# Performance work log

Hardware: AMD Instinct MI355X
Metric: run time of the kernel (lower is better)

The kernel has to match this reference:

```python
import jax, jax.numpy as jnp
import numpy as np

B, C, H, W = 16, 256, 64, 64
NUM_HEADS = 4
GROUPS = 8
EPS = 1e-5


def setup_inputs() -> dict:
    key = jax.random.key(0)
    ks = jax.random.split(key, 7)
    x = jax.random.normal(ks[0], (B, C, H, W), dtype=jnp.float32)
    # GroupNorm affine params (torch default: weight=1, bias=0; randomize slightly for a stronger test)
    norm_w = jnp.ones((C,), jnp.float32) + 0.1 * jax.random.normal(ks[1], (C,), jnp.float32)
    norm_b = 0.1 * jax.random.normal(ks[2], (C,), jnp.float32)
    # 1x1 convs == channel GEMMs; kaiming-uniform-ish init scale
    s = 1.0 / np.sqrt(C)
    qkv_w = jax.random.uniform(ks[3], (3 * C, C), jnp.float32, -s, s)
    qkv_b = jax.random.uniform(ks[4], (3 * C,), jnp.float32, -s, s)
    proj_w = jax.random.uniform(ks[5], (C, C), jnp.float32, -s, s)
    proj_b = jax.random.uniform(ks[6], (C,), jnp.float32, -s, s)
    return {"x": x, "norm_w": norm_w, "norm_b": norm_b,
            "qkv_w": qkv_w, "qkv_b": qkv_b, "proj_w": proj_w, "proj_b": proj_b}


def reference(x, norm_w, norm_b, qkv_w, qkv_b, proj_w, proj_b):
    b, c, h, w = x.shape
    nh = NUM_HEADS
    dh = c // nh
    n = h * w
    # GroupNorm(8, C)
    xg = x.reshape(b, GROUPS, c // GROUPS, h, w)
    mean = xg.mean(axis=(2, 3, 4), keepdims=True)
    var = xg.var(axis=(2, 3, 4), keepdims=True)
    xn = ((xg - mean) * jax.lax.rsqrt(var + EPS)).reshape(b, c, h, w)
    xn = xn * norm_w[None, :, None, None] + norm_b[None, :, None, None]
    # QKV 1x1 conv as channel GEMM
    qkv = jnp.einsum('bchw,oc->bohw', xn, qkv_w) + qkv_b[None, :, None, None]
    qkv = qkv.reshape(b, 3, nh, dh, n)
    q, k, v = qkv[:, 0], qkv[:, 1], qkv[:, 2]  # each (B, nh, dh, N)
    scale = dh ** (-0.5)
    # Faithful to original einsum labeling: contracts over spatial axis,
    # attention matrix is over the HEADS axis: attn (B, dh, nh, nh)
    attn = jnp.einsum('bnhd,bmhd->bhnm', q * scale, k)
    attn = jax.nn.softmax(attn, axis=-1)
    out = jnp.einsum('bhnm,bmhd->bnhd', attn, v).reshape(b, c, h, w)
    return jnp.einsum('bchw,oc->bohw', out, proj_w) + proj_b[None, :, None, None] + x
```

## Files before the change

kernel.cpp:

```cpp
#include <hip/hip_runtime.h>
#include <stdint.h>

#define BB 16
#define CC 256
#define PP 4096
#define CPG 32

typedef __attribute__((ext_vector_type(4))) float f32x4;
typedef __attribute__((ext_vector_type(8))) short bf16x8;

static __device__ __forceinline__ float bf2f(unsigned short u) {
    union { uint32_t i; float f; } w; w.i = ((uint32_t)u) << 16; return w.f;
}
static __device__ __forceinline__ unsigned short f2bf(float f) {
    union { float f; uint32_t i; } w; w.f = f;
    uint32_t u = w.i;
    uint32_t r = u + 0x7FFFu + ((u >> 16) & 1u);
    return (unsigned short)(r >> 16);
}

__global__ void gn_partial_k(const float* __restrict__ x, float* __restrict__ part) {
    int bg = blockIdx.x >> 2, chunk = blockIdx.x & 3;
    const f32x4* v = (const f32x4*)(x + (size_t)bg * (CPG * PP) + (size_t)chunk * (CPG * PP / 4));
    float s = 0.f, ss = 0.f;
    for (int i = threadIdx.x; i < (CPG * PP / 4 / 4); i += 256) {
        f32x4 t = v[i];
        s  += t.x + t.y + t.z + t.w;
        ss += t.x * t.x + t.y * t.y + t.z * t.z + t.w * t.w;
    }
    for (int off = 32; off > 0; off >>= 1) {
        s  += __shfl_down(s, off);
        ss += __shfl_down(ss, off);
    }
    __shared__ float ls[4], lss[4];
    int wv = threadIdx.x >> 6;
    if ((threadIdx.x & 63) == 0) { ls[wv] = s; lss[wv] = ss; }
    __syncthreads();
    if (threadIdx.x == 0) {
        part[blockIdx.x * 2 + 0] = ls[0] + ls[1] + ls[2] + ls[3];
        part[blockIdx.x * 2 + 1] = lss[0] + lss[1] + lss[2] + lss[3];
    }
}

__global__ void gn_final_k(const float* __restrict__ part, const float* __restrict__ nw,
                           const float* __restrict__ nb, float* __restrict__ a_s,
                           float* __restrict__ b_s) {
    int bg = threadIdx.x;
    float S = 0.f, SS = 0.f;
    for (int i = 0; i < 4; i++) { S += part[(bg * 4 + i) * 2]; SS += part[(bg * 4 + i) * 2 + 1]; }
    const float inv = 1.0f / (float)(CPG * PP);
    float mean = S * inv;
    float var = SS * inv - mean * mean;
    float rstd = rsqrtf(var + 1e-5f);
    int b = bg >> 3, g = bg & 7;
    for (int j = 0; j < CPG; j++) {
        int c = g * CPG + j;
        float w = nw[c];
        a_s[b * CC + c] = rstd * w;
        b_s[b * CC + c] = nb[c] - mean * rstd * w;
    }
}

__global__ void cvt_bf16_k(const float* __restrict__ in, unsigned short* __restrict__ out, int n) {
    int i = blockIdx.x * 256 + threadIdx.x;
    if (i < n) out[i] = f2bf(in[i]);
}

__global__ void xnt_k(const float* __restrict__ x, const float* __restrict__ a_s,
                      const float* __restrict__ b_s, unsigned short* __restrict__ xnT) {
    int pt = blockIdx.x & 63, ct = (blockIdx.x >> 6) & 3, b = blockIdx.x >> 8;
    int c0 = ct * 64, p0 = pt * 64;
    __shared__ unsigned short T[64][66];
    int t = threadIdx.x;
    int cl = t >> 4, pl4 = (t & 15) * 4;
    for (int i = 0; i < 4; i++) {
        int c = c0 + i * 16 + cl;
        float a = a_s[b * CC + c], sh = b_s[b * CC + c];
        f32x4 v = *(const f32x4*)(x + ((size_t)b * CC + c) * PP + p0 + pl4);
        T[i * 16 + cl][pl4 + 0] = f2bf(a * v.x + sh);
        T[i * 16 + cl][pl4 + 1] = f2bf(a * v.y + sh);
        T[i * 16 + cl][pl4 + 2] = f2bf(a * v.z + sh);
        T[i * 16 + cl][pl4 + 3] = f2bf(a * v.w + sh);
    }
    __syncthreads();
    int pl = t >> 2, c16 = (t & 3) * 16;
    union { unsigned short h[16]; uint4 u[2]; } buf;
    for (int j = 0; j < 16; j++) buf.h[j] = T[c16 + j][pl];
    unsigned short* dst = xnT + ((size_t)b * PP + p0 + pl) * CC + c0 + c16;
    *(uint4*)dst       = buf.u[0];
    *(uint4*)(dst + 8) = buf.u[1];
}

static __device__ __forceinline__ void gemm_core(const unsigned short* __restrict__ Aglob,
                                                 const unsigned short* __restrict__ Bglob,
                                                 f32x4 (&acc)[4][4]) {
    __shared__ unsigned short As[128][32];
    __shared__ unsigned short Bs[128][32];
    int t = threadIdx.x;
    int lane = t & 63, wave = t >> 6;
    int wm = wave >> 1, wn = wave & 1;
    int lr = lane & 15, lq = lane >> 4;
    int srow = t >> 2, sk8 = (t & 3) * 8;
    for (int mi = 0; mi < 4; mi++)
        for (int ni = 0; ni < 4; ni++) {
            acc[mi][ni][0] = 0.f; acc[mi][ni][1] = 0.f;
            acc[mi][ni][2] = 0.f; acc[mi][ni][3] = 0.f;
        }
    for (int k0 = 0; k0 < 256; k0 += 32) {
        uint4 av0 = *(const uint4*)(Aglob + (size_t)srow * 256 + k0 + sk8);
        uint4 av1 = *(const uint4*)(Aglob + (size_t)(srow + 64) * 256 + k0 + sk8);
        uint4 bv0 = *(const uint4*)(Bglob + (size_t)srow * 256 + k0 + sk8);
        uint4 bv1 = *(const uint4*)(Bglob + (size_t)(srow + 64) * 256 + k0 + sk8);
        __syncthreads();
        *(uint4*)&As[srow][sk8]      = av0;
        *(uint4*)&As[srow + 64][sk8] = av1;
        *(uint4*)&Bs[srow][sk8]      = bv0;
        *(uint4*)&Bs[srow + 64][sk8] = bv1;
        __syncthreads();
        bf16x8 af[4], bfr[4];
        for (int mi = 0; mi < 4; mi++) af[mi]  = *(const bf16x8*)&As[wm * 64 + mi * 16 + lr][lq * 8];
        for (int ni = 0; ni < 4; ni++) bfr[ni] = *(const bf16x8*)&Bs[wn * 64 + ni * 16 + lr][lq * 8];
        for (int mi = 0; mi < 4; mi++)
            for (int ni = 0; ni < 4; ni++)
                acc[mi][ni] = __builtin_amdgcn_mfma_f32_16x16x32_bf16(af[mi], bfr[ni], acc[mi][ni], 0, 0, 0);
    }
}

__global__ __launch_bounds__(256) void qkv_gemm_k(const unsigned short* __restrict__ Wq,
                                                  const unsigned short* __restrict__ xnT,
                                                  const float* __restrict__ qkv_b,
                                                  unsigned short* __restrict__ qk,
                                                  unsigned short* __restrict__ vT) {
    int nt = blockIdx.x & 31;
    int rest = blockIdx.x >> 5;
    int mt = rest % 6;
    int b  = rest / 6;
    int o0 = mt * 128, p0 = nt * 128;
    f32x4 acc[4][4];
    gemm_core(Wq + (size_t)o0 * 256, xnT + ((size_t)b * PP + p0) * 256, acc);
    int t = threadIdx.x, lane = t & 63, wave = t >> 6;
    int wm = wave >> 1, wn = wave & 1, lr = lane & 15, lq = lane >> 4;
    if (o0 < 512) {
        for (int mi = 0; mi < 4; mi++) {
            int ob = o0 + wm * 64 + mi * 16 + lq * 4;
            for (int ni = 0; ni < 4; ni++) {
                int p = p0 + wn * 64 + ni * 16 + lr;
                for (int r = 0; r < 4; r++) {
                    int o = ob + r;
                    qk[((size_t)b * 512 + o) * PP + p] = f2bf(acc[mi][ni][r] + qkv_b[o]);
                }
            }
        }
    } else {
        for (int mi = 0; mi < 4; mi++) {
            int cb = (o0 - 512) + wm * 64 + mi * 16 + lq * 4;
            for (int ni = 0; ni < 4; ni++) {
                int p = p0 + wn * 64 + ni * 16 + lr;
                for (int r = 0; r < 4; r++) {
                    int c = cb + r;
                    vT[((size_t)b * PP + p) * CC + c] = f2bf(acc[mi][ni][r] + qkv_b[512 + c]);
                }
            }
        }
    }
}

__global__ void scores_k(const unsigned short* __restrict__ qk, float* __restrict__ attn) {
    int b = blockIdx.x >> 6, hh = blockIdx.x & 63;
    int t = threadIdx.x, lane = t & 63, wave = t >> 6;
    float acc[16];
    for (int i = 0; i < 16; i++) acc[i] = 0.f;
    const unsigned short* qb = qk + (size_t)b * 512 * PP + (size_t)hh * PP;
    for (int p = t * 4; p < PP; p += 1024) {
        float qv[4][4], kv[4][4];
        for (int n = 0; n < 4; n++) {
            ushort4 u = *(const ushort4*)(qb + (size_t)n * 64 * PP + p);
            qv[n][0] = bf2f(u.x); qv[n][1] = bf2f(u.y); qv[n][2] = bf2f(u.z); qv[n][3] = bf2f(u.w);
        }
        for (int m = 0; m < 4; m++) {
            ushort4 u = *(const ushort4*)(qb + (size_t)(256 + m * 64) * PP + p);
            kv[m][0] = bf2f(u.x); kv[m][1] = bf2f(u.y); kv[m][2] = bf2f(u.z); kv[m][3] = bf2f(u.w);
        }
        for (int n = 0; n < 4; n++)
            for (int m = 0; m < 4; m++)
                acc[n * 4 + m] += qv[n][0] * kv[m][0] + qv[n][1] * kv[m][1] +
                                  qv[n][2] * kv[m][2] + qv[n][3] * kv[m][3];
    }
    __shared__ float red[4][16];
    __shared__ float sfin[16];
    for (int i = 0; i < 16; i++) {
        float v = acc[i];
        for (int off = 32; off > 0; off >>= 1) v += __shfl_down(v, off);
        if (lane == 0) red[wave][i] = v;
    }
    __syncthreads();
    if (t < 16) sfin[t] = red[0][t] + red[1][t] + red[2][t] + red[3][t];
    __syncthreads();
    if (t < 4) {
        float v0 = sfin[t * 4 + 0] * 0.125f, v1 = sfin[t * 4 + 1] * 0.125f;
        float v2 = sfin[t * 4 + 2] * 0.125f, v3 = sfin[t * 4 + 3] * 0.125f;
        float mx = fmaxf(fmaxf(v0, v1), fmaxf(v2, v3));
        float e0 = expf(v0 - mx), e1 = expf(v1 - mx), e2 = expf(v2 - mx), e3 = expf(v3 - mx);
        float inv = 1.0f / (e0 + e1 + e2 + e3);
        float* dst = attn + ((size_t)(b * 64 + hh) * 4 + t) * 4;
        dst[0] = e0 * inv; dst[1] = e1 * inv; dst[2] = e2 * inv; dst[3] = e3 * inv;
    }
}

__global__ void make_wp_k(const float* __restrict__ proj_w, const float* __restrict__ attn,
                          unsigned short* __restrict__ Wp) {
    int t = threadIdx.x;
    int o = blockIdx.x & 255, b = blockIdx.x >> 8;
    int m = t >> 6, hh = t & 63;
    float s = 0.f;
    for (int n = 0; n < 4; n++)
        s += proj_w[o * 256 + n * 64 + hh] * attn[((size_t)(b * 64 + hh) * 4 + n) * 4 + m];
    Wp[((size_t)b * 256 + o) * 256 + t] = f2bf(s);
}

__global__ __launch_bounds__(256) void final_gemm_k(const unsigned short* __restrict__ Wp,
                                                    const unsigned short* __restrict__ vT,
                                                    const float* __restrict__ proj_b,
                                                    const float* __restrict__ x,
                                                    float* __restrict__ out) {
    int nt = blockIdx.x & 31;
    int rest = blockIdx.x >> 5;
    int mt = rest & 1;
    int b  = rest >> 1;
    int o0 = mt * 128, p0 = nt * 128;
    f32x4 acc[4][4];
    gemm_core(Wp + ((size_t)b * 256 + o0) * 256, vT + ((size_t)b * PP + p0) * 256, acc);
    int t = threadIdx.x, lane = t & 63, wave = t >> 6;
    int wm = wave >> 1, wn = wave & 1, lr = lane & 15, lq = lane >> 4;
    for (int mi = 0; mi < 4; mi++) {
        int ob = o0 + wm * 64 + mi * 16 + lq * 4;
        for (int ni = 0; ni < 4; ni++) {
            int p = p0 + wn * 64 + ni * 16 + lr;
            for (int r = 0; r < 4; r++) {
                int o = ob + r;
                size_t idx = ((size_t)b * CC + o) * PP + p;
                out[idx] = acc[mi][ni][r] + proj_b[o] + x[idx];
            }
        }
    }
}

extern "C" void kernel_launch(void* const* d_in, const int* in_sizes, int n_in,
                              void* d_out, int out_size, void* d_ws, size_t ws_size,
                              hipStream_t stream) {
    const float* x      = (const float*)d_in[0];
    const float* norm_w = (const float*)d_in[1];
    const float* norm_b = (const float*)d_in[2];
    const float* qkv_w  = (const float*)d_in[3];
    const float* qkv_b  = (const float*)d_in[4];
    const float* proj_w = (const float*)d_in[5];
    const float* proj_b = (const float*)d_in[6];
    float* out = (float*)d_out;

    char* ws = (char*)d_ws;
    size_t off = 0;
    auto alloc = [&](size_t bytes) {
        void* p = ws + off;
        off += (bytes + 255) & ~(size_t)255;
        return p;
    };
    float* part = (float*)alloc(512 * 2 * sizeof(float));
    float* a_s  = (float*)alloc(BB * CC * sizeof(float));
    float* b_s  = (float*)alloc(BB * CC * sizeof(float));
    float* attn = (float*)alloc((size_t)BB * 64 * 16 * sizeof(float));
    unsigned short* Wqb = (unsigned short*)alloc((size_t)768 * 256 * 2);
    unsigned short* Wp  = (unsigned short*)alloc((size_t)BB * 256 * 256 * 2);
    unsigned short* xnT = (unsigned short*)alloc((size_t)BB * PP * CC * 2);
    unsigned short* qk  = (unsigned short*)alloc((size_t)BB * 512 * PP * 2);
    unsigned short* vT  = (unsigned short*)alloc((size_t)BB * PP * CC * 2);

    gn_partial_k<<<512, 256, 0, stream>>>(x, part);
    gn_final_k<<<1, 128, 0, stream>>>(part, norm_w, norm_b, a_s, b_s);
    cvt_bf16_k<<<768, 256, 0, stream>>>(qkv_w, Wqb, 768 * 256);
    xnt_k<<<4096, 256, 0, stream>>>(x, a_s, b_s, xnT);
    qkv_gemm_k<<<16 * 6 * 32, 256, 0, stream>>>(Wqb, xnT, qkv_b, qk, vT);
    scores_k<<<16 * 64, 256, 0, stream>>>(qk, attn);
    make_wp_k<<<16 * 256, 256, 0, stream>>>(proj_w, attn, Wp);
    final_gemm_k<<<16 * 2 * 32, 256, 0, stream>>>(Wp, vT, proj_b, x, out);
}
```

Before: 292.7 us.

## Use direct global-to-LDS loads and swap GEMM operands for vectorized epilogue stores

The shared GEMM core now stages tiles with global_load_lds, so data goes straight into LDS without a round trip through registers. For the qk and final GEMMs the operands are swapped, which puts each lane's four accumulator values on consecutive spatial positions; the epilogues can then write 4-wide ushort4/float4 stores and read the residual x as a float4 instead of issuing scalar strided writes. The scores kernel also widens its loads to 16 bytes. A risk is that global_load_lds requires LDS addresses to follow the lane-contiguous layout, and the loop keeps its single-buffer barriers.

Result: faster. 283.5 us (-3.1%).

```diff
diff --git a/kernel.cpp b/kernel.cpp
--- a/kernel.cpp
+++ b/kernel.cpp
@@ -17,6 +17,12 @@
     uint32_t u = w.i;
     uint32_t r = u + 0x7FFFu + ((u >> 16) & 1u);
     return (unsigned short)(r >> 16);
+}
+
+static __device__ __forceinline__ void gl2lds16(const void* g, void* l) {
+    __builtin_amdgcn_global_load_lds(
+        (const __attribute__((address_space(1))) void*)g,
+        (__attribute__((address_space(3))) void*)l, 16, 0, 0);
 }
 
 __global__ void gn_partial_k(const float* __restrict__ x, float* __restrict__ part) {
@@ -91,11 +97,11 @@
     *(uint4*)(dst + 8) = buf.u[1];
 }
 
-static __device__ __forceinline__ void gemm_core(const unsigned short* __restrict__ Aglob,
-                                                 const unsigned short* __restrict__ Bglob,
+static __device__ __forceinline__ void gemm_core(const unsigned short* __restrict__ Rg,
+                                                 const unsigned short* __restrict__ Cg,
                                                  f32x4 (&acc)[4][4]) {
-    __shared__ unsigned short As[128][32];
-    __shared__ unsigned short Bs[128][32];
+    __shared__ unsigned short Rs[128][32];
+    __shared__ unsigned short Cs[128][32];
     int t = threadIdx.x;
     int lane = t & 63, wave = t >> 6;
     int wm = wave >> 1, wn = wave & 1;
@@ -106,20 +112,24 @@
             acc[mi][ni][0] = 0.f; acc[mi][ni][1] = 0.f;
             acc[mi][ni][2] = 0.f; acc[mi][ni][3] = 0.f;
         }
+    const unsigned short* gr0 = Rg + (size_t)srow * 256 + sk8;
+    const unsigned short* gr1 = gr0 + (size_t)64 * 256;
+    const unsigned short* gc0 = Cg + (size_t)srow * 256 + sk8;
+    const unsigned short* gc1 = gc0 + (size_t)64 * 256;
+    char* lr0 = (char*)&Rs[0][0] + t * 16;
+    char* lr1 = lr0 + 4096;
+    char* lc0 = (char*)&Cs[0][0] + t * 16;
+    char* lc1 = lc0 + 4096;
     for (int k0 = 0; k0 < 256; k0 += 32) {
-        uint4 av0 = *(const uint4*)(Aglob + (size_t)srow * 256 + k0 + sk8);
-        uint4 av1 = *(const uint4*)(Aglob + (size_t)(srow + 64) * 256 + k0 + sk8);
-        uint4 bv0 = *(const uint4*)(Bglob + (size_t)srow * 256 + k0 + sk8);
-        uint4 bv1 = *(const uint4*)(Bglob + (size_t)(srow + 64) * 256 + k0 + sk8);
         __syncthreads();
-        *(uint4*)&As[srow][sk8]      = av0;
-        *(uint4*)&As[srow + 64][sk8] = av1;
-        *(uint4*)&Bs[srow][sk8]      = bv0;
-        *(uint4*)&Bs[srow + 64][sk8] = bv1;
+        gl2lds16(gr0 + k0, lr0);
+        gl2lds16(gr1 + k0, lr1);
+        gl2lds16(gc0 + k0, lc0);
+        gl2lds16(gc1 + k0, lc1);
         __syncthreads();
         bf16x8 af[4], bfr[4];
-        for (int mi = 0; mi < 4; mi++) af[mi]  = *(const bf16x8*)&As[wm * 64 + mi * 16 + lr][lq * 8];
-        for (int ni = 0; ni < 4; ni++) bfr[ni] = *(const bf16x8*)&Bs[wn * 64 + ni * 16 + lr][lq * 8];
+        for (int mi = 0; mi < 4; mi++) af[mi]  = *(const bf16x8*)&Rs[wm * 64 + mi * 16 + lr][lq * 8];
+        for (int ni = 0; ni < 4; ni++) bfr[ni] = *(const bf16x8*)&Cs[wn * 64 + ni * 16 + lr][lq * 8];
         for (int mi = 0; mi < 4; mi++)
             for (int ni = 0; ni < 4; ni++)
                 acc[mi][ni] = __builtin_amdgcn_mfma_f32_16x16x32_bf16(af[mi], bfr[ni], acc[mi][ni], 0, 0, 0);
@@ -136,30 +146,36 @@
     int mt = rest % 6;
     int b  = rest / 6;
     int o0 = mt * 128, p0 = nt * 128;
-    f32x4 acc[4][4];
-    gemm_core(Wq + (size_t)o0 * 256, xnT + ((size_t)b * PP + p0) * 256, acc);
     int t = threadIdx.x, lane = t & 63, wave = t >> 6;
     int wm = wave >> 1, wn = wave & 1, lr = lane & 15, lq = lane >> 4;
+    f32x4 acc[4][4];
     if (o0 < 512) {
+        gemm_core(xnT + ((size_t)b * PP + p0) * 256, Wq + (size_t)o0 * 256, acc);
         for (int mi = 0; mi < 4; mi++) {
-            int ob = o0 + wm * 64 + mi * 16 + lq * 4;
+            int p4 = p0 + wm * 64 + mi * 16 + lq * 4;
+            for (int ni = 0; ni < 4; ni++) {
+                int o = o0 + wn * 64 + ni * 16 + lr;
+                float bias = qkv_b[o];
+                ushort4 u;
+                u.x = f2bf(acc[mi][ni][0] + bias);
+                u.y = f2bf(acc[mi][ni][1] + bias);
+                u.z = f2bf(acc[mi][ni][2] + bias);
+                u.w = f2bf(acc[mi][ni][3] + bias);
+                *(ushort4*)(qk + ((size_t)b * 512 + o) * PP + p4) = u;
+            }
+        }
+    } else {
+        gemm_core(Wq + (size_t)o0 * 256, xnT + ((size_t)b * PP + p0) * 256, acc);
+        for (int mi = 0; mi < 4; mi++) {
+            int c4 = (o0 - 512) + wm * 64 + mi * 16 + lq * 4;
             for (int ni = 0; ni < 4; ni++) {
                 int p = p0 + wn * 64 + ni * 16 + lr;
-                for (int r = 0; r < 4; r++) {
-                    int o = ob + r;
-                    qk[((size_t)b * 512 + o) * PP + p] = f2bf(acc[mi][ni][r] + qkv_b[o]);
-                }
-            }
-        }
-    } else {
-        for (int mi = 0; mi < 4; mi++) {
-            int cb = (o0 - 512) + wm * 64 + mi * 16 + lq * 4;
-            for (int ni = 0; ni < 4; ni++) {
-                int p = p0 + wn * 64 + ni * 16 + lr;
-                for (int r = 0; r < 4; r++) {
-                    int c = cb + r;
-                    vT[((size_t)b * PP + p) * CC + c] = f2bf(acc[mi][ni][r] + qkv_b[512 + c]);
-                }
+                ushort4 u;
+                u.x = f2bf(acc[mi][ni][0] + qkv_b[512 + c4 + 0]);
+                u.y = f2bf(acc[mi][ni][1] + qkv_b[512 + c4 + 1]);
+                u.z = f2bf(acc[mi][ni][2] + qkv_b[512 + c4 + 2]);
+                u.w = f2bf(acc[mi][ni][3] + qkv_b[512 + c4 + 3]);
+                *(ushort4*)(vT + ((size_t)b * PP + p) * CC + c4) = u;
             }
         }
     }
@@ -171,20 +187,24 @@
     float acc[16];
     for (int i = 0; i < 16; i++) acc[i] = 0.f;
     const unsigned short* qb = qk + (size_t)b * 512 * PP + (size_t)hh * PP;
-    for (int p = t * 4; p < PP; p += 1024) {
-        float qv[4][4], kv[4][4];
+    for (int p = t * 8; p < PP; p += 2048) {
+        float qv[4][8], kv[4][8];
         for (int n = 0; n < 4; n++) {
-            ushort4 u = *(const ushort4*)(qb + (size_t)n * 64 * PP + p);
-            qv[n][0] = bf2f(u.x); qv[n][1] = bf2f(u.y); qv[n][2] = bf2f(u.z); qv[n][3] = bf2f(u.w);
+            uint4 u = *(const uint4*)(qb + (size_t)n * 64 * PP + p);
+            const unsigned short* hs = (const unsigned short*)&u;
+            for (int j = 0; j < 8; j++) qv[n][j] = bf2f(hs[j]);
         }
         for (int m = 0; m < 4; m++) {
-            ushort4 u = *(const ushort4*)(qb + (size_t)(256 + m * 64) * PP + p);
-            kv[m][0] = bf2f(u.x); kv[m][1] = bf2f(u.y); kv[m][2] = bf2f(u.z); kv[m][3] = bf2f(u.w);
+            uint4 u = *(const uint4*)(qb + (size_t)(256 + m * 64) * PP + p);
+            const unsigned short* hs = (const unsigned short*)&u;
+            for (int j = 0; j < 8; j++) kv[m][j] = bf2f(hs[j]);
         }
         for (int n = 0; n < 4; n++)
-            for (int m = 0; m < 4; m++)
-                acc[n * 4 + m] += qv[n][0] * kv[m][0] + qv[n][1] * kv[m][1] +
-                                  qv[n][2] * kv[m][2] + qv[n][3] * kv[m][3];
+            for (int m = 0; m < 4; m++) {
+                float s = 0.f;
+                for (int j = 0; j < 8; j++) s += qv[n][j] * kv[m][j];
+                acc[n * 4 + m] += s;
+            }
     }
     __shared__ float red[4][16];
     __shared__ float sfin[16];
@@ -229,18 +249,22 @@
     int b  = rest >> 1;
     int o0 = mt * 128, p0 = nt * 128;
     f32x4 acc[4][4];
-    gemm_core(Wp + ((size_t)b * 256 + o0) * 256, vT + ((size_t)b * PP + p0) * 256, acc);
+    gemm_core(vT + ((size_t)b * PP + p0) * 256, Wp + ((size_t)b * 256 + o0) * 256, acc);
     int t = threadIdx.x, lane = t & 63, wave = t >> 6;
     int wm = wave >> 1, wn = wave & 1, lr = lane & 15, lq = lane >> 4;
     for (int mi = 0; mi < 4; mi++) {
-        int ob = o0 + wm * 64 + mi * 16 + lq * 4;
+        int p4 = p0 + wm * 64 + mi * 16 + lq * 4;
         for (int ni = 0; ni < 4; ni++) {
-            int p = p0 + wn * 64 + ni * 16 + lr;
-            for (int r = 0; r < 4; r++) {
-                int o = ob + r;
-                size_t idx = ((size_t)b * CC + o) * PP + p;
-                out[idx] = acc[mi][ni][r] + proj_b[o] + x[idx];
-            }
+            int o = o0 + wn * 64 + ni * 16 + lr;
+            size_t idx = ((size_t)b * CC + o) * PP + p4;
+            float bias = proj_b[o];
+            f32x4 xv = *(const f32x4*)(x + idx);
+            f32x4 r;
+            r[0] = acc[mi][ni][0] + bias + xv[0];
+            r[1] = acc[mi][ni][1] + bias + xv[1];
+            r[2] = acc[mi][ni][2] + bias + xv[2];
+            r[3] = acc[mi][ni][3] + bias + xv[3];
+            *(f32x4*)(out + idx) = r;
         }
     }
 }
```
